# Kernel tuning notes

Hardware: AMD Instinct MI355X
Metric: run time of the kernel (lower is better)

The kernel has to match this reference:

```python
import jax, jax.numpy as jnp
import numpy as np

B, T, N, D = 8, 64, 196, 768
K, P = 8, 2
BOUND = 2.5
EPS = 1e-6


def _dct2_basis(T, P, dtype=jnp.float32):
    t = jnp.arange(T, dtype=dtype) + 0.5
    rows = [jnp.ones(T, dtype=dtype)]
    for p in range(1, P + 1):
        rows.append(jnp.cos(jnp.pi * p * t / T))
    Bm = jnp.stack(rows, axis=0)  # [P+1, T]
    return Bm / (jnp.sqrt(jnp.sum(Bm * Bm, axis=1, keepdims=True)) + EPS)


def setup_inputs() -> dict:
    key = jax.random.key(0)
    k1, k2, k3 = jax.random.split(key, 3)
    x = jax.random.normal(k1, (B, T, N, D), dtype=jnp.float32)
    valid_mask = jnp.ones((B, T, N), dtype=jnp.float32)
    # proj weight [K, D]; module orthonormalizes (QR of W.T) every forward,
    # so we materialize the already-orthonormalized parameter value here.
    W0 = jax.random.uniform(k2, (K, D), dtype=jnp.float32, minval=-0.05, maxval=0.05)
    Q, _ = jnp.linalg.qr(W0.T)          # [D, K] orthonormal cols
    proj_W = Q.T                         # [K, D]
    feat_in = K * (P + 3)                # K*(P+1+2) = 40
    bound = float(np.sqrt(6.0 / (feat_in + D)))
    W_raw = jax.random.uniform(k3, (feat_in, D), dtype=jnp.float32, minval=-bound, maxval=bound)
    beta = jnp.full((D,), 0.5, dtype=jnp.float32)
    return {"x": x, "valid_mask": valid_mask, "proj_W": proj_W, "W_raw": W_raw, "beta": beta}


def reference(x, valid_mask, proj_W, W_raw, beta):
    b, t, n, d = x.shape
    U = proj_W.T                                         # [D, K]
    v = jnp.einsum('btnd,dk->btnk', x, U)
    v = v * valid_mask[..., None]
    v_bnkt = jnp.transpose(v, (0, 2, 3, 1))              # [B, N, K, T]
    rms = jnp.sqrt(jnp.mean(v_bnkt * v_bnkt, axis=-1, keepdims=True) + EPS)
    v_bounded = BOUND * jnp.tanh(v_bnkt / (rms + EPS))
    Bmat = _dct2_basis(t, P, x.dtype)                    # [P+1, T]
    coeff = jnp.einsum('bnkt,pt->bnkp', v_bounded, Bmat)
    mean_feat = jnp.mean(v_bounded, axis=-1, keepdims=True)
    rms_feat = jnp.sqrt(jnp.mean(v_bounded * v_bounded, axis=-1, keepdims=True) + EPS)
    feats = jnp.concatenate([coeff, mean_feat, rms_feat], axis=-1).reshape(b, n, -1)  # [B,N,K*(P+3)]
    W = jax.nn.softplus(W_raw)                           # [feat_in, D]
    y = feats @ W                                        # [B, N, D]
    beta_s = jax.nn.sigmoid(beta)[None, None, None, :]
    h = x + beta_s * y[:, None, :, :]
    m = valid_mask[..., None]
    h = m * h + (1.0 - m) * x
    return (h, W)
```

## Files before the change

### kernel.cpp

```cpp
#include <hip/hip_runtime.h>
#include <math.h>

#define B_ 8
#define T_ 64
#define N_ 196
#define D_ 768
#define K_ 8
#define FEAT 40
#define EPSF 1e-6f

constexpr int BN = B_ * N_;
constexpr int ROWS = B_ * T_ * N_;
constexpr long long HSIZE = (long long)ROWS * D_;
constexpr int QPR = D_ / 4;
constexpr unsigned RSTRIDE = (unsigned)N_ * QPR;

typedef float v4f __attribute__((ext_vector_type(4)));

__device__ __forceinline__ float wredux(float v) {
#pragma unroll
    for (int off = 32; off > 0; off >>= 1)
        v += __shfl_xor(v, off, 64);
    return v;
}

__device__ __forceinline__ float dot4(v4f a, v4f b) {
    return a.x * b.x + a.y * b.y + a.z * b.z + a.w * b.w;
}

__global__ __launch_bounds__(256) void k_wsp(const float* __restrict__ wraw,
                                             const float* __restrict__ beta,
                                             float* __restrict__ wout,
                                             float* __restrict__ beta_s) {
    int i = blockIdx.x * blockDim.x + threadIdx.x;
    if (i < FEAT * D_) {
        float xw = wraw[i];
        wout[i] = fmaxf(xw, 0.0f) + log1pf(expf(-fabsf(xw)));
    }
    if (i < D_) beta_s[i] = 1.0f / (1.0f + expf(-beta[i]));
}

__global__ __launch_bounds__(256)
void k_fused(const float* __restrict__ x,
             const float* __restrict__ mask,
             const float* __restrict__ pw,
             const float* __restrict__ wsp,
             const float* __restrict__ beta_s,
             float* __restrict__ h) {
    __shared__ v4f   xbuf[2][4][QPR];
    __shared__ float vpart[T_][K_ + 1];
    __shared__ float sf[FEAT];
    __shared__ float ylds[D_];
    __shared__ float smask[T_];

    const int tid  = threadIdx.x;
    const int lane = tid & 63;
    const int w    = tid >> 6;
    const int bn   = blockIdx.x;
    const int b    = bn / N_;
    const int n    = bn - b * N_;

    v4f u[2][3];
#pragma unroll
    for (int kk = 0; kk < 2; kk++)
#pragma unroll
        for (int c = 0; c < 3; c++)
            u[kk][c] = *(const v4f*)(pw + (2 * w + kk) * D_ + c * 256 + lane * 4);

    if (tid < T_) smask[tid] = mask[(b * T_ + tid) * N_ + n];

    const v4f* x4 = (const v4f*)x;
    const unsigned TSTRIDE = 4 * RSTRIDE;
    unsigned q = (unsigned)((b * T_ + w) * N_ + n) * QPR;
    v4f R0 = x4[q + lane], R1 = x4[q + 64 + lane], R2 = x4[q + 128 + lane];
    xbuf[0][w][lane]       = R0;
    xbuf[0][w][64 + lane]  = R1;
    xbuf[0][w][128 + lane] = R2;
    __syncthreads();
    int p = 0;
#pragma unroll 1
    for (int tile = 0; tile < 16; ++tile) {
        if (tile < 15) {
            q += TSTRIDE;
            R0 = x4[q + lane];
            R1 = x4[q + 64 + lane];
            R2 = x4[q + 128 + lane];
        }
#pragma unroll
        for (int r = 0; r < 4; ++r) {
            v4f c0 = xbuf[p][r][lane];
            v4f c1 = xbuf[p][r][64 + lane];
            v4f c2 = xbuf[p][r][128 + lane];
            float a0 = dot4(c0, u[0][0]) + dot4(c1, u[0][1]) + dot4(c2, u[0][2]);
            float a1 = dot4(c0, u[1][0]) + dot4(c1, u[1][1]) + dot4(c2, u[1][2]);
            a0 += __shfl_xor(a0, 1, 64);
            a1 += __shfl_xor(a1, 1, 64);
            float val = (lane & 1) ? a1 : a0;
            val += __shfl_xor(val, 2, 64);
            val += __shfl_xor(val, 4, 64);
            val += __shfl_xor(val, 8, 64);
            val += __shfl_xor(val, 16, 64);
            val += __shfl_xor(val, 32, 64);
            if (lane < 2) vpart[tile * 4 + r][2 * w + lane] = val;
        }
        if (tile < 15) {
            xbuf[p ^ 1][w][lane]       = R0;
            xbuf[p ^ 1][w][64 + lane]  = R1;
            xbuf[p ^ 1][w][128 + lane] = R2;
        }
        __syncthreads();
        p ^= 1;
    }

#pragma unroll
    for (int kk = 0; kk < 2; kk++) {
        const int k = w + kk * 4;
        float v = vpart[lane][k] * smask[lane];
        float s2  = wredux(v * v);
        float rms = sqrtf(s2 * (1.0f / T_) + EPSF);
        float vb  = 2.5f * tanhf(v / (rms + EPSF));
        const float PI = 3.14159265358979323846f;
        float ph = PI * ((float)lane + 0.5f) / (float)T_;
        float c1 = cosf(ph), c2 = cosf(2.0f * ph);
        float n1 = wredux(c1 * c1), n2 = wredux(c2 * c2);
        float S1 = wredux(vb), Sc1 = wredux(vb * c1);
        float Sc2 = wredux(vb * c2), Sq = wredux(vb * vb);
        if (lane == 0) {
            float* o = sf + k * 5;
            o[0] = S1 / (8.0f + EPSF);
            o[1] = Sc1 / (sqrtf(n1) + EPSF);
            o[2] = Sc2 / (sqrtf(n2) + EPSF);
            o[3] = S1 * (1.0f / T_);
            o[4] = sqrtf(Sq * (1.0f / T_) + EPSF);
        }
    }
    __syncthreads();

    for (int d = tid; d < D_; d += 256) {
        float a0 = 0.f, a1 = 0.f;
#pragma unroll
        for (int f = 0; f < FEAT; f += 2) {
            a0 += sf[f]     * wsp[f * D_ + d];
            a1 += sf[f + 1] * wsp[(f + 1) * D_ + d];
        }
        ylds[d] = (a0 + a1) * beta_s[d];
    }
    __syncthreads();

    const v4f* y4 = (const v4f*)ylds;
    const v4f y0 = y4[lane], y1 = y4[64 + lane], y2 = y4[128 + lane];
    v4f* h4 = (v4f*)h;
    unsigned qD = (unsigned)((b * T_ + w * 16) * N_ + n) * QPR;
    v4f d0 = __builtin_nontemporal_load(x4 + qD + lane);
    v4f d1 = __builtin_nontemporal_load(x4 + qD + 64 + lane);
    v4f d2 = __builtin_nontemporal_load(x4 + qD + 128 + lane);
#pragma unroll 1
    for (int j = 0; j < 16; j++) {
        v4f c0 = d0, c1 = d1, c2 = d2;
        const unsigned qc = qD;
        if (j < 15) {
            qD += RSTRIDE;
            d0 = __builtin_nontemporal_load(x4 + qD + lane);
            d1 = __builtin_nontemporal_load(x4 + qD + 64 + lane);
            d2 = __builtin_nontemporal_load(x4 + qD + 128 + lane);
        }
        const float m = smask[w * 16 + j];
        __builtin_nontemporal_store(c0 + m * y0, h4 + qc + lane);
        __builtin_nontemporal_store(c1 + m * y1, h4 + qc + 64 + lane);
        __builtin_nontemporal_store(c2 + m * y2, h4 + qc + 128 + lane);
    }
}

extern "C" void kernel_launch(void* const* d_in, const int* in_sizes, int n_in,
                              void* d_out, int out_size, void* d_ws, size_t ws_size,
                              hipStream_t stream) {
    const float* x    = (const float*)d_in[0];
    const float* mask = (const float*)d_in[1];
    const float* pw   = (const float*)d_in[2];
    const float* wraw = (const float*)d_in[3];
    const float* beta = (const float*)d_in[4];

    float* h    = (float*)d_out;
    float* wout = h + HSIZE;
    float* beta_s = (float*)d_ws;

    hipLaunchKernelGGL(k_wsp, dim3((FEAT * D_ + 255) / 256), dim3(256), 0, stream,
                       wraw, beta, wout, beta_s);
    hipLaunchKernelGGL(k_fused, dim3(BN), dim3(256), 0, stream,
                       x, mask, pw, wout, beta_s, h);
}
```

Measured before the change: 151.5 us.

## Process two (b,n) columns per block, overlapping first output write with second projection

Each block now handles two consecutive (b,n) columns. The output write for the first column is interleaved with the x streaming for the second column's projection, and the x reads in that pass switch from nontemporal to normal loads. The aim is to hide the serial phases (feature reduction, feature-to-output matvec) behind memory traffic and to raise per-block work. The trade-off is half as many blocks, 784 instead of 1568, which may reduce latency hiding across CUs, plus more LDS and code size.

New measurement: 206.6 us. +36.4%, slower.

```diff
diff --git a/kernel.cpp b/kernel.cpp
--- a/kernel.cpp
+++ b/kernel.cpp
@@ -14,6 +14,7 @@
 constexpr long long HSIZE = (long long)ROWS * D_;
 constexpr int QPR = D_ / 4;
 constexpr unsigned RSTRIDE = (unsigned)N_ * QPR;
+constexpr unsigned TSTRIDE = 4 * RSTRIDE;
 
 typedef float v4f __attribute__((ext_vector_type(4)));
 
@@ -50,15 +51,16 @@
     __shared__ v4f   xbuf[2][4][QPR];
     __shared__ float vpart[T_][K_ + 1];
     __shared__ float sf[FEAT];
-    __shared__ float ylds[D_];
-    __shared__ float smask[T_];
+    __shared__ float ylds[2][D_];
+    __shared__ float smask[2][T_];
 
     const int tid  = threadIdx.x;
     const int lane = tid & 63;
     const int w    = tid >> 6;
-    const int bn   = blockIdx.x;
-    const int b    = bn / N_;
-    const int n    = bn - b * N_;
+    const int c0   = 2 * blockIdx.x;
+    const int c1   = c0 + 1;
+    const int b0   = c0 / N_, n0 = c0 - b0 * N_;
+    const int b1   = c1 / N_, n1 = c1 - b1 * N_;
 
     v4f u[2][3];
 #pragma unroll
@@ -67,11 +69,17 @@
         for (int c = 0; c < 3; c++)
             u[kk][c] = *(const v4f*)(pw + (2 * w + kk) * D_ + c * 256 + lane * 4);
 
-    if (tid < T_) smask[tid] = mask[(b * T_ + tid) * N_ + n];
+    if (tid < T_) {
+        smask[0][tid] = mask[(b0 * T_ + tid) * N_ + n0];
+        smask[1][tid] = mask[(b1 * T_ + tid) * N_ + n1];
+    }
 
     const v4f* x4 = (const v4f*)x;
-    const unsigned TSTRIDE = 4 * RSTRIDE;
-    unsigned q = (unsigned)((b * T_ + w) * N_ + n) * QPR;
+    v4f* h4 = (v4f*)h;
+    const unsigned qbase0 = (unsigned)((b0 * T_) * N_ + n0) * QPR;
+    const unsigned qbase1 = (unsigned)((b1 * T_) * N_ + n1) * QPR;
+
+    unsigned q = qbase0 + w * RSTRIDE;
     v4f R0 = x4[q + lane], R1 = x4[q + 64 + lane], R2 = x4[q + 128 + lane];
     xbuf[0][w][lane]       = R0;
     xbuf[0][w][64 + lane]  = R1;
@@ -88,11 +96,11 @@
         }
 #pragma unroll
         for (int r = 0; r < 4; ++r) {
-            v4f c0 = xbuf[p][r][lane];
-            v4f c1 = xbuf[p][r][64 + lane];
-            v4f c2 = xbuf[p][r][128 + lane];
-            float a0 = dot4(c0, u[0][0]) + dot4(c1, u[0][1]) + dot4(c2, u[0][2]);
-            float a1 = dot4(c0, u[1][0]) + dot4(c1, u[1][1]) + dot4(c2, u[1][2]);
+            v4f c0v = xbuf[p][r][lane];
+            v4f c1v = xbuf[p][r][64 + lane];
+            v4f c2v = xbuf[p][r][128 + lane];
+            float a0 = dot4(c0v, u[0][0]) + dot4(c1v, u[0][1]) + dot4(c2v, u[0][2]);
+            float a1 = dot4(c0v, u[1][0]) + dot4(c1v, u[1][1]) + dot4(c2v, u[1][2]);
             a0 += __shfl_xor(a0, 1, 64);
             a1 += __shfl_xor(a1, 1, 64);
             float val = (lane & 1) ? a1 : a0;
@@ -112,24 +120,27 @@
         p ^= 1;
     }
 
+    q = qbase1 + w * RSTRIDE;
+    R0 = x4[q + lane]; R1 = x4[q + 64 + lane]; R2 = x4[q + 128 + lane];
+
 #pragma unroll
     for (int kk = 0; kk < 2; kk++) {
         const int k = w + kk * 4;
-        float v = vpart[lane][k] * smask[lane];
+        float v = vpart[lane][k] * smask[0][lane];
         float s2  = wredux(v * v);
         float rms = sqrtf(s2 * (1.0f / T_) + EPSF);
         float vb  = 2.5f * tanhf(v / (rms + EPSF));
         const float PI = 3.14159265358979323846f;
         float ph = PI * ((float)lane + 0.5f) / (float)T_;
-        float c1 = cosf(ph), c2 = cosf(2.0f * ph);
-        float n1 = wredux(c1 * c1), n2 = wredux(c2 * c2);
-        float S1 = wredux(vb), Sc1 = wredux(vb * c1);
-        float Sc2 = wredux(vb * c2), Sq = wredux(vb * vb);
+        float cc1 = cosf(ph), cc2 = cosf(2.0f * ph);
+        float nn1 = wredux(cc1 * cc1), nn2 = wredux(cc2 * cc2);
+        float S1 = wredux(vb), Sc1 = wredux(vb * cc1);
+        float Sc2 = wredux(vb * cc2), Sq = wredux(vb * vb);
         if (lane == 0) {
             float* o = sf + k * 5;
             o[0] = S1 / (8.0f + EPSF);
-            o[1] = Sc1 / (sqrtf(n1) + EPSF);
-            o[2] = Sc2 / (sqrtf(n2) + EPSF);
+            o[1] = Sc1 / (sqrtf(nn1) + EPSF);
+            o[2] = Sc2 / (sqrtf(nn2) + EPSF);
             o[3] = S1 * (1.0f / T_);
             o[4] = sqrtf(Sq * (1.0f / T_) + EPSF);
         }
@@ -143,31 +154,116 @@
             a0 += sf[f]     * wsp[f * D_ + d];
             a1 += sf[f + 1] * wsp[(f + 1) * D_ + d];
         }
-        ylds[d] = (a0 + a1) * beta_s[d];
-    }
-    __syncthreads();
-
-    const v4f* y4 = (const v4f*)ylds;
-    const v4f y0 = y4[lane], y1 = y4[64 + lane], y2 = y4[128 + lane];
-    v4f* h4 = (v4f*)h;
-    unsigned qD = (unsigned)((b * T_ + w * 16) * N_ + n) * QPR;
-    v4f d0 = __builtin_nontemporal_load(x4 + qD + lane);
-    v4f d1 = __builtin_nontemporal_load(x4 + qD + 64 + lane);
-    v4f d2 = __builtin_nontemporal_load(x4 + qD + 128 + lane);
+        ylds[0][d] = (a0 + a1) * beta_s[d];
+    }
+    __syncthreads();
+
+    xbuf[0][w][lane]       = R0;
+    xbuf[0][w][64 + lane]  = R1;
+    xbuf[0][w][128 + lane] = R2;
+    __syncthreads();
+    p = 0;
+    unsigned qd = qbase0 + w * RSTRIDE;
+    const v4f* y0p = (const v4f*)ylds[0];
+#pragma unroll 1
+    for (int tile = 0; tile < 16; ++tile) {
+        if (tile < 15) {
+            q += TSTRIDE;
+            R0 = x4[q + lane];
+            R1 = x4[q + 64 + lane];
+            R2 = x4[q + 128 + lane];
+        }
+#pragma unroll
+        for (int r = 0; r < 4; ++r) {
+            v4f c0v = xbuf[p][r][lane];
+            v4f c1v = xbuf[p][r][64 + lane];
+            v4f c2v = xbuf[p][r][128 + lane];
+            float a0 = dot4(c0v, u[0][0]) + dot4(c1v, u[0][1]) + dot4(c2v, u[0][2]);
+            float a1 = dot4(c0v, u[1][0]) + dot4(c1v, u[1][1]) + dot4(c2v, u[1][2]);
+            a0 += __shfl_xor(a0, 1, 64);
+            a1 += __shfl_xor(a1, 1, 64);
+            float val = (lane & 1) ? a1 : a0;
+            val += __shfl_xor(val, 2, 64);
+            val += __shfl_xor(val, 4, 64);
+            val += __shfl_xor(val, 8, 64);
+            val += __shfl_xor(val, 16, 64);
+            val += __shfl_xor(val, 32, 64);
+            if (lane < 2) vpart[tile * 4 + r][2 * w + lane] = val;
+        }
+        {
+            v4f e0 = x4[qd + lane];
+            v4f e1 = x4[qd + 64 + lane];
+            v4f e2 = x4[qd + 128 + lane];
+            const float m = smask[0][tile * 4 + w];
+            __builtin_nontemporal_store(e0 + m * y0p[lane],        h4 + qd + lane);
+            __builtin_nontemporal_store(e1 + m * y0p[64 + lane],   h4 + qd + 64 + lane);
+            __builtin_nontemporal_store(e2 + m * y0p[128 + lane],  h4 + qd + 128 + lane);
+            qd += TSTRIDE;
+        }
+        if (tile < 15) {
+            xbuf[p ^ 1][w][lane]       = R0;
+            xbuf[p ^ 1][w][64 + lane]  = R1;
+            xbuf[p ^ 1][w][128 + lane] = R2;
+        }
+        __syncthreads();
+        p ^= 1;
+    }
+
+#pragma unroll
+    for (int kk = 0; kk < 2; kk++) {
+        const int k = w + kk * 4;
+        float v = vpart[lane][k] * smask[1][lane];
+        float s2  = wredux(v * v);
+        float rms = sqrtf(s2 * (1.0f / T_) + EPSF);
+        float vb  = 2.5f * tanhf(v / (rms + EPSF));
+        const float PI = 3.14159265358979323846f;
+        float ph = PI * ((float)lane + 0.5f) / (float)T_;
+        float cc1 = cosf(ph), cc2 = cosf(2.0f * ph);
+        float nn1 = wredux(cc1 * cc1), nn2 = wredux(cc2 * cc2);
+        float S1 = wredux(vb), Sc1 = wredux(vb * cc1);
+        float Sc2 = wredux(vb * cc2), Sq = wredux(vb * vb);
+        if (lane == 0) {
+            float* o = sf + k * 5;
+            o[0] = S1 / (8.0f + EPSF);
+            o[1] = Sc1 / (sqrtf(nn1) + EPSF);
+            o[2] = Sc2 / (sqrtf(nn2) + EPSF);
+            o[3] = S1 * (1.0f / T_);
+            o[4] = sqrtf(Sq * (1.0f / T_) + EPSF);
+        }
+    }
+    __syncthreads();
+
+    for (int d = tid; d < D_; d += 256) {
+        float a0 = 0.f, a1 = 0.f;
+#pragma unroll
+        for (int f = 0; f < FEAT; f += 2) {
+            a0 += sf[f]     * wsp[f * D_ + d];
+            a1 += sf[f + 1] * wsp[(f + 1) * D_ + d];
+        }
+        ylds[1][d] = (a0 + a1) * beta_s[d];
+    }
+    __syncthreads();
+
+    const v4f* y1p = (const v4f*)ylds[1];
+    const v4f y0 = y1p[lane], y1 = y1p[64 + lane], y2 = y1p[128 + lane];
+    unsigned qD = qbase1 + (unsigned)(w * 16) * RSTRIDE;
+    v4f d0 = x4[qD + lane];
+    v4f d1 = x4[qD + 64 + lane];
+    v4f d2 = x4[qD + 128 + lane];
 #pragma unroll 1
     for (int j = 0; j < 16; j++) {
-        v4f c0 = d0, c1 = d1, c2 = d2;
+        v4f e0 = d0, e1 = d1, e2 = d2;
         const unsigned qc = qD;
         if (j < 15) {
             qD += RSTRIDE;
-            d0 = __builtin_nontemporal_load(x4 + qD + lane);
-            d1 = __builtin_nontemporal_load(x4 + qD + 64 + lane);
-            d2 = __builtin_nontemporal_load(x4 + qD + 128 + lane);
-        }
-        const float m = smask[w * 16 + j];
-        __builtin_nontemporal_store(c0 + m * y0, h4 + qc + lane);
-        __builtin_nontemporal_store(c1 + m * y1, h4 + qc + 64 + lane);
-        __builtin_nontemporal_store(c2 + m * y2, h4 + qc + 128 + lane);
+            d0 = x4[qD + lane];
+            d1 = x4[qD + 64 + lane];
+            d2 = x4[qD + 128 + lane];
+        }
+        const float m = smask[1][w * 16 + j];
+        __builtin_nontemporal_store(e0 + m * y0, h4 + qc + lane);
+        __builtin_nontemporal_store(e1 + m * y1, h4 + qc + 64 + lane);
+        __builtin_nontemporal_store(e2 + m * y2, h4 + qc + 128 + lane);
     }
 }
 
@@ -186,6 +282,6 @@
 
     hipLaunchKernelGGL(k_wsp, dim3((FEAT * D_ + 255) / 256), dim3(256), 0, stream,
                        wraw, beta, wout, beta_s);
-    hipLaunchKernelGGL(k_fused, dim3(BN), dim3(256), 0, stream,
+    hipLaunchKernelGGL(k_fused, dim3(BN / 2), dim3(256), 0, stream,
                        x, mask, pw, wout, beta_s, h);
 }
```
